# Kernel optimization log

Hardware: AMD Instinct MI355X
Metric: run time of the kernel (lower is better)

Reference implementation:

```python
import jax, jax.numpy as jnp
import numpy as np

DIM = 768
HEADS = 12
HEAD_DIM = DIM // HEADS  # 64, must equal 2*ROPE_DIM
HIDDEN = int(DIM * 4 * 2 / 3)  # 2048
EPS = 1e-6


def _ln(x, w, b, eps=EPS):
    mu = jnp.mean(x, -1, keepdims=True)
    var = jnp.mean((x - mu) ** 2, -1, keepdims=True)
    return (x - mu) * jax.lax.rsqrt(var + eps) * w + b


def _rotate_half(x):
    xr = x.reshape(x.shape[:-1] + (-1, 2))
    return jnp.stack((-xr[..., 1], xr[..., 0]), -1).reshape(x.shape)


def _rope_tables(H, W):
    # Matches get_rope: dim=32 per axis, pt_seq_len=16, theta=10000
    dim, pt, theta = 32, 16.0, 10000.0
    freqs = 1.0 / theta ** (np.arange(0, dim, 2, dtype=np.float32) / dim)  # [16]
    fH = np.repeat((np.arange(H, dtype=np.float32) / H * pt)[:, None] * freqs[None, :], 2, axis=-1)  # [H,32]
    fW = np.repeat((np.arange(W, dtype=np.float32) / W * pt)[:, None] * freqs[None, :], 2, axis=-1)  # [W,32]
    f = np.concatenate([np.broadcast_to(fH[:, None, :], (H, W, dim)),
                        np.broadcast_to(fW[None, :, :], (H, W, dim))], -1)  # [H,W,64]
    f = f.reshape(H * W, 2 * dim)
    return jnp.asarray(np.cos(f)), jnp.asarray(np.sin(f))


def block_forward(x, ln1_w, ln1_b, q_w, q_b, k_w, v_w, v_b, proj_w, proj_b,
                  ln2_w, ln2_b, w1_w, w1_b, w2_w, w2_b, ffn_w, ffn_b, w3_w, w3_b, ws):
    B, H, W, C = x.shape
    shortcut = x
    h = _ln(x, ln1_w, ln1_b)
    # window partition with padding
    pad_h = (-H) % ws
    pad_w = (-W) % ws
    h = jnp.pad(h, ((0, 0), (0, pad_h), (0, pad_w), (0, 0)))
    Hp, Wp = H + pad_h, W + pad_w
    h = h.reshape(B, Hp // ws, ws, Wp // ws, ws, C).transpose(0, 1, 3, 2, 4, 5).reshape(-1, ws, ws, C)
    Bw = h.shape[0]
    N = ws * ws
    t = h.reshape(Bw, N, C)
    q = t @ q_w + q_b  # k has no bias
    k = t @ k_w
    v = t @ v_w + v_b
    q = q.reshape(Bw, N, HEADS, HEAD_DIM).transpose(0, 2, 1, 3)  # [Bw,h,N,d]
    k = k.reshape(Bw, N, HEADS, HEAD_DIM).transpose(0, 2, 1, 3)
    v = v.reshape(Bw, N, HEADS, HEAD_DIM).transpose(0, 2, 1, 3)
    cos, sin = _rope_tables(ws, ws)  # [N, 64]
    q = q * cos + _rotate_half(q) * sin
    k = k * cos + _rotate_half(k) * sin
    scale = HEAD_DIM ** (-0.5)
    attn = jax.nn.softmax(jnp.einsum('bhnd,bhmd->bhnm', q * scale, k), axis=-1)
    o = jnp.einsum('bhnm,bhmd->bhnd', attn, v).transpose(0, 2, 1, 3).reshape(Bw, N, -1)
    o = o @ proj_w + proj_b
    o = o.reshape(Bw, ws, ws, C)
    # window unpartition
    o = o.reshape(B, Hp // ws, Wp // ws, ws, ws, C).transpose(0, 1, 3, 2, 4, 5).reshape(B, Hp, Wp, C)
    o = o[:, :H, :W, :]
    x = shortcut + o
    # SwiGLU MLP with sub-LN
    h = _ln(x, ln2_w, ln2_b)
    hid = jax.nn.silu(h @ w1_w + w1_b) * (h @ w2_w + w2_b)
    hid = _ln(hid, ffn_w, ffn_b)
    return x + hid @ w3_w + w3_b


def setup_inputs() -> dict:
    key = jax.random.key(0)
    ks = jax.random.split(key, 9)
    s = 0.02
    d = {
        'x': jax.random.normal(ks[0], (8, 64, 64, DIM), jnp.float32),
        'ln1_w': jnp.ones((DIM,), jnp.float32),
        'ln1_b': jnp.zeros((DIM,), jnp.float32),
        'q_w': jax.random.normal(ks[1], (DIM, DIM), jnp.float32) * s,
        'q_b': jnp.zeros((DIM,), jnp.float32),
        'k_w': jax.random.normal(ks[2], (DIM, DIM), jnp.float32) * s,
        'v_w': jax.random.normal(ks[3], (DIM, DIM), jnp.float32) * s,
        'v_b': jnp.zeros((DIM,), jnp.float32),
        'proj_w': jax.random.normal(ks[4], (DIM, DIM), jnp.float32) * s,
        'proj_b': jnp.zeros((DIM,), jnp.float32),
        'ln2_w': jnp.ones((DIM,), jnp.float32),
        'ln2_b': jnp.zeros((DIM,), jnp.float32),
        'w1_w': jax.random.normal(ks[5], (DIM, HIDDEN), jnp.float32) * s,
        'w1_b': jnp.zeros((HIDDEN,), jnp.float32),
        'w2_w': jax.random.normal(ks[6], (DIM, HIDDEN), jnp.float32) * s,
        'w2_b': jnp.zeros((HIDDEN,), jnp.float32),
        'ffn_w': jnp.ones((HIDDEN,), jnp.float32),
        'ffn_b': jnp.zeros((HIDDEN,), jnp.float32),
        'w3_w': jax.random.normal(ks[7], (HIDDEN, DIM), jnp.float32) * s,
        'w3_b': jnp.zeros((DIM,), jnp.float32),
        'window_size': 14,
    }
    return d


def reference(x, ln1_w, ln1_b, q_w, q_b, k_w, v_w, v_b, proj_w, proj_b,
              ln2_w, ln2_b, w1_w, w1_b, w2_w, w2_b, ffn_w, ffn_b, w3_w, w3_b, window_size):
    return block_forward(x, ln1_w, ln1_b, q_w, q_b, k_w, v_w, v_b, proj_w, proj_b,
                         ln2_w, ln2_b, w1_w, w1_b, w2_w, w2_b, ffn_w, ffn_b, w3_w, w3_b,
                         int(window_size))
```

## Files before the change

kernel.cpp:

```cpp
#include <hip/hip_runtime.h>
#include <hip/hip_bf16.h>
#include <stdint.h>

typedef unsigned short u16;
typedef unsigned int u32;
typedef __attribute__((ext_vector_type(4))) float f32x4;
typedef __attribute__((ext_vector_type(8))) short s16x8;
typedef __attribute__((ext_vector_type(4))) u32 u32x4;

#define DEV __device__ __forceinline__
#define AS1 __attribute__((address_space(1)))
#define AS3 __attribute__((address_space(3)))

constexpr int T2 = 8 * 64 * 64;
constexpr int C = 768;
constexpr int HID = 2048;
constexpr int CHUNK = 16384;
constexpr int QKVS = 2304;

DEV float blo(u32 u) { return __uint_as_float(u << 16); }
DEV float bhi(u32 u) { return __uint_as_float(u & 0xffff0000u); }
DEV u16 f2bf(float f) {
  u32 x = __float_as_uint(f);
  u32 r = x + 0x7fffu + ((x >> 16) & 1u);
  return (u16)(r >> 16);
}
DEV u32 pack2(float a, float b) { return (u32)f2bf(a) | ((u32)f2bf(b) << 16); }
DEV u32 cvtpk(float lo, float hi) {
  u32 r;
  asm("v_cvt_pk_bf16_f32 %0, %1, %2" : "=v"(r) : "v"(lo), "v"(hi));
  return r;
}

DEV void reduce2(float& s, float& q) {
#pragma unroll
  for (int o = 32; o > 0; o >>= 1) {
    s += __shfl_down(s, o);
    q += __shfl_down(q, o);
  }
  __shared__ float ps[8];
  int wave = threadIdx.x >> 6, lane = threadIdx.x & 63;
  if (lane == 0) { ps[wave] = s; ps[4 + wave] = q; }
  __syncthreads();
  s = ps[0] + ps[1] + ps[2] + ps[3];
  q = ps[4] + ps[5] + ps[6] + ps[7];
}

__global__ __launch_bounds__(256) void transpose_cvt_tiled_k(
    const float* __restrict__ src, u16* __restrict__ dst, int K, int N, int rs, int ro) {
  __shared__ float t[32][33];
  int k0 = blockIdx.x * 32, n0 = blockIdx.y * 32;
  int tx = threadIdx.x, ty = threadIdx.y;
#pragma unroll
  for (int j = 0; j < 4; ++j)
    t[ty + j * 8][tx] = src[(size_t)(k0 + ty + j * 8) * N + n0 + tx];
  __syncthreads();
#pragma unroll
  for (int j = 0; j < 4; ++j) {
    int n = n0 + ty + j * 8;
    dst[((size_t)n * rs + ro) * K + k0 + tx] = f2bf(t[tx][ty + j * 8]);
  }
}

__global__ void build_biases_k(const float* __restrict__ qb, const float* __restrict__ vbb,
                               const float* __restrict__ w1b, const float* __restrict__ w2b,
                               float* __restrict__ qkvb, float* __restrict__ w12b) {
  int i = blockIdx.x * 256 + threadIdx.x;
  if (i < 2304)
    qkvb[i] = i < 768 ? qb[i] : (i < 1536 ? 0.f : vbb[i - 1536]);
  int j = i - 2304;
  if (j >= 0 && j < 4096) w12b[j] = (j & 1) ? w2b[j >> 1] : w1b[j >> 1];
}

__global__ void rope_tables_k(float* __restrict__ ct, float* __restrict__ st) {
  int i = blockIdx.x * 256 + threadIdx.x;
  if (i >= 196 * 32) return;
  int n = i >> 5, jp = i & 31;
  int d = jp << 1;
  int r = n / 14, c = n - r * 14;
  float pos, fj;
  if (d < 32) { pos = (float)r * (16.f / 14.f); fj = (float)(d >> 1); }
  else        { pos = (float)c * (16.f / 14.f); fj = (float)((d - 32) >> 1); }
  float fr = __expf(fj * (-2.f / 32.f) * logf(10000.f));
  float ang = pos * fr;
  float cv = cosf(ang), sv = sinf(ang);
  ct[n * 64 + d] = cv; ct[n * 64 + d + 1] = cv;
  st[n * 64 + d] = sv; st[n * 64 + d + 1] = sv;
}

__global__ __launch_bounds__(256) void ln_k(const float* __restrict__ in,
    const float* __restrict__ w, const float* __restrict__ bb, u16* __restrict__ out) {
  size_t row = blockIdx.x;
  int tid = threadIdx.x;
  const float* xr = in + row * C;
  float v0 = xr[tid], v1 = xr[tid + 256], v2 = xr[tid + 512];
  float s = v0 + v1 + v2, q = v0 * v0 + v1 * v1 + v2 * v2;
  reduce2(s, q);
  float mu = s * (1.f / 768.f), var = q * (1.f / 768.f) - mu * mu;
  float rs = rsqrtf(var + 1e-6f);
  u16* orow = out + row * C;
  orow[tid]       = f2bf((v0 - mu) * rs * w[tid]       + bb[tid]);
  orow[tid + 256] = f2bf((v1 - mu) * rs * w[tid + 256] + bb[tid + 256]);
  orow[tid + 512] = f2bf((v2 - mu) * rs * w[tid + 512] + bb[tid + 512]);
}

DEV float rope1(float v, float p, int r, int d, bool odd, bool isq,
                const float* __restrict__ ct, const float* __restrict__ st) {
  int rem = r & 4095;
  int n = ((rem >> 6) % 14) * 14 + ((rem & 63) % 14);
  float c = ct[n * 64 + d], s = st[n * 64 + d];
  float o = odd ? (v * c + p * s) : (v * c - p * s);
  return isq ? o * 0.125f : o;
}

template <int EPI>
__global__ __launch_bounds__(256) void gemm_k(
    const u16* __restrict__ A, const u16* __restrict__ Bt,
    const float* __restrict__ bias, void* __restrict__ Cout,
    const float* __restrict__ resid, int M, int Nn, int K, int lda,
    const float* __restrict__ ct, const float* __restrict__ st) {
  __shared__ u16 As[128 * 64];
  __shared__ u16 Bs[128 * 64];
  const int tid = threadIdx.x;
  const int wave = tid >> 6, lane = tid & 63;
  const int wm = wave >> 1, wn = wave & 1;
  const int gx = gridDim.x;
  const int id = blockIdx.y * gx + blockIdx.x;
  const int xcd = id & 7;
  const int j0 = id >> 3;
  const int per_sub = gridDim.y << 4;
  const int sub = j0 / per_sub;
  const int jj = j0 - sub * per_sub;
  const int tm = xcd * (gx >> 3) + (sub << 4) + (jj & 15);
  const int tn = jj >> 4;
  const int l16 = lane & 15, lq = lane >> 4;

  f32x4 acc[4][4];
#pragma unroll
  for (int a = 0; a < 4; ++a)
#pragma unroll
    for (int b = 0; b < 4; ++b)
#pragma unroll
      for (int e = 0; e < 4; ++e) acc[a][b][e] = 0.f;

  const int nk = K >> 6;
  for (int kt = 0; kt < nk; ++kt) {
    const int k0 = kt << 6;
#pragma unroll
    for (int i = 0; i < 4; ++i) {
      int row = (((wave << 2) + i) << 3) + (lane >> 3);
      int cl = (lane & 7) ^ (row & 7);
      const u16* sa = A + (size_t)(tm * 128 + row) * lda + k0 + cl * 8;
      __builtin_amdgcn_global_load_lds((const AS1 u32*)sa,
          (AS3 u32*)(As + (((wave << 2) + i) << 9)), 16, 0, 0);
      const u16* sb = Bt + (size_t)(tn * 128 + row) * K + k0 + cl * 8;
      __builtin_amdgcn_global_load_lds((const AS1 u32*)sb,
          (AS3 u32*)(Bs + (((wave << 2) + i) << 9)), 16, 0, 0);
    }
    asm volatile("s_waitcnt vmcnt(0)" ::: "memory");
    __syncthreads();
#pragma unroll
    for (int ks = 0; ks < 2; ++ks) {
      s16x8 af[4], bfr[4];
#pragma unroll
      for (int mf = 0; mf < 4; ++mf) {
        int row = (wm << 6) + (mf << 4) + l16;
        int sc = ((ks << 2) + lq) ^ (row & 7);
        af[mf] = *(const s16x8*)(As + row * 64 + sc * 8);
      }
#pragma unroll
      for (int nf = 0; nf < 4; ++nf) {
        int row = (wn << 6) + (nf << 4) + l16;
        int sc = ((ks << 2) + lq) ^ (row & 7);
        bfr[nf] = *(const s16x8*)(Bs + row * 64 + sc * 8);
      }
      __builtin_amdgcn_s_setprio(1);
#pragma unroll
      for (int mf = 0; mf < 4; ++mf)
#pragma unroll
        for (int nf = 0; nf < 4; ++nf)
          acc[mf][nf] =
              __builtin_amdgcn_mfma_f32_16x16x32_bf16(af[mf], bfr[nf], acc[mf][nf], 0, 0, 0);
      __builtin_amdgcn_s_setprio(0);
    }
    __syncthreads();
  }

#pragma unroll
  for (int nf = 0; nf < 4; ++nf) {
    int col = (tn << 7) + (wn << 6) + (nf << 4) + l16;
    float bs = bias ? bias[col] : 0.f;
#pragma unroll
    for (int mf = 0; mf < 4; ++mf) {
      int rbase = (tm << 7) + (wm << 6) + (mf << 4) + (lq << 2);
      if constexpr (EPI == 0 || EPI == 3) {
        float v[4];
#pragma unroll
        for (int j = 0; j < 4; ++j) v[j] = acc[mf][nf][j] + bs;
        if constexpr (EPI == 3) {
          float pv[4];
#pragma unroll
          for (int j = 0; j < 4; ++j) pv[j] = __shfl_xor(v[j], 1);
          if (col < 1536) {
            bool odd = (l16 & 1) != 0, isq = col < 768;
            int d = col & 63;
#pragma unroll
            for (int j = 0; j < 4; ++j)
              v[j] = rope1(v[j], pv[j], rbase + j, d, odd, isq, ct, st);
          }
        }
        u32 p01 = cvtpk(v[0], v[1]);
        u32 p23 = cvtpk(v[2], v[3]);
        u16* cp = (u16*)Cout + (size_t)rbase * Nn + col;
        cp[0] = (u16)p01;
        cp[Nn] = (u16)(p01 >> 16);
        cp[2 * Nn] = (u16)p23;
        cp[3 * Nn] = (u16)(p23 >> 16);
      } else {
#pragma unroll
        for (int j = 0; j < 4; ++j) {
          size_t idx = (size_t)(rbase + j) * Nn + col;
          ((float*)Cout)[idx] = resid[idx] + acc[mf][nf][j] + bs;
        }
      }
    }
  }
}

__global__ __launch_bounds__(256) void attn_mfma_k(u16* __restrict__ qkv,
    const float* __restrict__ vb) {
  __shared__ u16 Vt[64 * 224];
  __shared__ u16 Pl[4 * 16 * 40];
  __shared__ int rowTab[208];
  int wid = blockIdx.x / 12, h = blockIdx.x - wid * 12;
  int bi = wid / 25, wr = wid - bi * 25;
  int hi = wr / 5, wj = wr - hi * 5;
  int rh = (hi == 4) ? 8 : 14, rw = (wj == 4) ? 8 : 14;
  int nv = rh * rw;
  int nk16 = (nv + 15) >> 4;
  int kvfull = nk16 >> 1;
  int nsteps = kvfull + (nk16 & 1);
  int vcols = ((nk16 + 1) >> 1) << 5;
  int tid = threadIdx.x;
  int rowbase = (bi * 64 + hi * 14) * 64 + wj * 14;

  if (tid < 208) {
    int mk = tid < nv ? tid : nv - 1;
    int nr = mk / rw, nc = mk - nr * rw;
    rowTab[tid] = rowbase + nr * 64 + nc;
  }
  __syncthreads();
  for (int idx = tid; idx < vcols * 32; idx += 256) {
    int key = idx >> 5, dp = idx & 31;
    int d = dp << 1;
    u32 val;
    if (key < nv) {
      size_t off = (size_t)rowTab[key] * QKVS + 1536 + (h << 6) + d;
      val = *(const u32*)(qkv + off);
    } else {
      val = pack2(vb[(h << 6) + d], vb[(h << 6) + d + 1]);
    }
    int b0 = (d * 448 + key * 2) ^ ((d & 7) << 4);
    int b1 = ((d + 1) * 448 + key * 2) ^ (((d + 1) & 7) << 4);
    Vt[b0 >> 1] = (u16)(val & 0xffffu);
    Vt[b1 >> 1] = (u16)(val >> 16);
  }
  __syncthreads();

  int wave = tid >> 6, lane = tid & 63;
  int l16 = lane & 15, lq = lane >> 4;
  u16* Pw = Pl + wave * 640;
  const u16* kbase = qkv + 768 + (h << 6);
  float vbr[4];
#pragma unroll
  for (int dt = 0; dt < 4; ++dt) vbr[dt] = vb[(h << 6) + dt * 16 + l16];

  int mtiles = (nv + 15) >> 4;
  for (int mt = wave; mt < mtiles; mt += 4) {
    s16x8 a[2];
    {
      int qi = mt * 16 + l16;
      const u16* qp = qkv + (size_t)rowTab[qi] * QKVS + (h << 6);
      a[0] = *(const s16x8*)(qp + lq * 8);
      a[1] = *(const s16x8*)(qp + 32 + lq * 8);
    }
    f32x4 O[4];
#pragma unroll
    for (int dt = 0; dt < 4; ++dt)
#pragma unroll
      for (int j = 0; j < 4; ++j) O[dt][j] = 0.f;
    float lrow[4] = {0.f, 0.f, 0.f, 0.f};

    for (int kv = 0; kv < nsteps; ++kv) {
      const bool full = kv < kvfull;
      const int keyb = kv << 5;
      f32x4 s0 = {0.f, 0.f, 0.f, 0.f}, s1 = {0.f, 0.f, 0.f, 0.f};
      int key0 = keyb + l16, key1 = key0 + 16;
      const u16* kr0 = kbase + (size_t)rowTab[key0] * QKVS;
      const u16* kr1 = full ? (kbase + (size_t)rowTab[key1] * QKVS) : kbase;
      __builtin_amdgcn_s_setprio(1);
#pragma unroll
      for (int s = 0; s < 2; ++s) {
        s16x8 b0 = *(const s16x8*)(kr0 + s * 32 + lq * 8);
        s0 = __builtin_amdgcn_mfma_f32_16x16x32_bf16(a[s], b0, s0, 0, 0, 0);
        if (full) {
          s16x8 b1 = *(const s16x8*)(kr1 + s * 32 + lq * 8);
          s1 = __builtin_amdgcn_mfma_f32_16x16x32_bf16(a[s], b1, s1, 0, 0, 0);
        }
      }
      __builtin_amdgcn_s_setprio(0);
#pragma unroll
      for (int j = 0; j < 4; ++j) {
        float p0 = key0 < nv ? __expf(s0[j]) : (key0 < 196 ? 1.f : 0.f);
        float p1 = full ? (key1 < nv ? __expf(s1[j]) : (key1 < 196 ? 1.f : 0.f)) : 0.f;
        float rs = p0 + p1;
        rs += __shfl_xor(rs, 1);
        rs += __shfl_xor(rs, 2);
        rs += __shfl_xor(rs, 4);
        rs += __shfl_xor(rs, 8);
        lrow[j] += rs;
        u32 pk = cvtpk(p0, p1);
        Pw[(lq * 4 + j) * 40 + l16] = (u16)pk;
        Pw[(lq * 4 + j) * 40 + l16 + 16] = (u16)(pk >> 16);
      }
      s16x8 pa = *(const s16x8*)(Pw + l16 * 40 + lq * 8);
      __builtin_amdgcn_s_setprio(1);
#pragma unroll
      for (int dt = 0; dt < 4; ++dt) {
        int d = dt * 16 + l16;
        int vbyte = (d * 448 + keyb * 2 + lq * 16) ^ ((d & 7) << 4);
        s16x8 bv = *(const s16x8*)(Vt + (vbyte >> 1));
        O[dt] = __builtin_amdgcn_mfma_f32_16x16x32_bf16(pa, bv, O[dt], 0, 0, 0);
      }
      __builtin_amdgcn_s_setprio(0);
    }
    int Prem = 196 - (nk16 << 4);
    if (Prem > 0) {
#pragma unroll
      for (int j = 0; j < 4; ++j) {
        lrow[j] += (float)Prem;
#pragma unroll
        for (int dt = 0; dt < 4; ++dt) O[dt][j] += (float)Prem * vbr[dt];
      }
    }
#pragma unroll
    for (int j = 0; j < 4; ++j) {
      int qi = mt * 16 + lq * 4 + j;
      if (qi < nv) {
        float inv = 1.f / lrow[j];
        u16* op = qkv + (size_t)rowTab[qi] * QKVS + (h << 6);
#pragma unroll
        for (int dt = 0; dt < 4; ++dt) op[dt * 16 + l16] = f2bf(O[dt][j] * inv);
      }
    }
  }
}

__global__ __launch_bounds__(256) void swiglu_ln_k(u16* __restrict__ h12,
    const float* __restrict__ w, const float* __restrict__ bb) {
  size_t row = blockIdx.x;
  int tid = threadIdx.x;
  const u32x4 ua = *(const u32x4*)(h12 + row * 4096 + tid * 16);
  const u32x4 ub = *(const u32x4*)(h12 + row * 4096 + tid * 16 + 8);
  u32 pp[8] = {ua.x, ua.y, ua.z, ua.w, ub.x, ub.y, ub.z, ub.w};
  float g[8];
  float s = 0.f, qq = 0.f;
#pragma unroll
  for (int j = 0; j < 8; ++j) {
    float a = blo(pp[j]), b = bhi(pp[j]);
    float sl = a / (1.f + __expf(-a));
    g[j] = sl * b;
    s += g[j];
    qq += g[j] * g[j];
  }
  reduce2(s, qq);
  float mu = s * (1.f / 2048.f);
  float var = qq * (1.f / 2048.f) - mu * mu;
  float rs = rsqrtf(var + 1e-6f);
  const float* wp = w + tid * 8;
  const float* bp = bb + tid * 8;
  u32 o4[4];
#pragma unroll
  for (int j = 0; j < 4; ++j) {
    float o0 = (g[2 * j] - mu) * rs * wp[2 * j] + bp[2 * j];
    float o1 = (g[2 * j + 1] - mu) * rs * wp[2 * j + 1] + bp[2 * j + 1];
    o4[j] = cvtpk(o0, o1);
  }
  *(u32x4*)(h12 + row * 4096 + tid * 8) = (u32x4){o4[0], o4[1], o4[2], o4[3]};
}

extern "C" void kernel_launch(void* const* d_in, const int* in_sizes, int n_in,
                              void* d_out, int out_size, void* d_ws, size_t ws_size,
                              hipStream_t stream) {
  const float* x    = (const float*)d_in[0];
  const float* ln1w = (const float*)d_in[1];
  const float* ln1b = (const float*)d_in[2];
  const float* qw   = (const float*)d_in[3];
  const float* qb   = (const float*)d_in[4];
  const float* kw   = (const float*)d_in[5];
  const float* vw   = (const float*)d_in[6];
  const float* vb   = (const float*)d_in[7];
  const float* pw   = (const float*)d_in[8];
  const float* pb   = (const float*)d_in[9];
  const float* ln2w = (const float*)d_in[10];
  const float* ln2b = (const float*)d_in[11];
  const float* w1   = (const float*)d_in[12];
  const float* w1b  = (const float*)d_in[13];
  const float* w2   = (const float*)d_in[14];
  const float* w2b  = (const float*)d_in[15];
  const float* ffw  = (const float*)d_in[16];
  const float* ffb  = (const float*)d_in[17];
  const float* w3   = (const float*)d_in[18];
  const float* w3b  = (const float*)d_in[19];

  char* ws = (char*)d_ws;
  size_t off = 0;
  auto alloc = [&](size_t bytes) -> char* {
    char* p = ws + off;
    off += (bytes + 255) & ~(size_t)255;
    return p;
  };
  u16* qkvwt = (u16*)alloc((size_t)QKVS * 768 * 2);
  u16* pwt   = (u16*)alloc((size_t)768 * 768 * 2);
  u16* w12t  = (u16*)alloc((size_t)4096 * 768 * 2);
  u16* w3t   = (u16*)alloc((size_t)768 * 2048 * 2);
  float* qkvb = (float*)alloc((size_t)QKVS * 4);
  float* w12b = (float*)alloc((size_t)4096 * 4);
  float* ct = (float*)alloc((size_t)196 * 64 * 4);
  float* st = (float*)alloc((size_t)196 * 64 * 4);
  u16* xw  = (u16*)alloc((size_t)T2 * C * 2);
  u16* qkv = (u16*)alloc((size_t)T2 * QKVS * 2);
  u16* h12c = qkv;
  float* x2 = (float*)d_out;

  dim3 tb(32, 8);
  transpose_cvt_tiled_k<<<dim3(24, 24), tb, 0, stream>>>(qw, qkvwt, 768, 768, 1, 0);
  transpose_cvt_tiled_k<<<dim3(24, 24), tb, 0, stream>>>(kw, qkvwt + (size_t)768 * 768, 768, 768, 1, 0);
  transpose_cvt_tiled_k<<<dim3(24, 24), tb, 0, stream>>>(vw, qkvwt + (size_t)1536 * 768, 768, 768, 1, 0);
  transpose_cvt_tiled_k<<<dim3(24, 24), tb, 0, stream>>>(pw, pwt, 768, 768, 1, 0);
  transpose_cvt_tiled_k<<<dim3(24, 64), tb, 0, stream>>>(w1, w12t, 768, 2048, 2, 0);
  transpose_cvt_tiled_k<<<dim3(24, 64), tb, 0, stream>>>(w2, w12t, 768, 2048, 2, 1);
  transpose_cvt_tiled_k<<<dim3(64, 24), tb, 0, stream>>>(w3, w3t, 2048, 768, 1, 0);
  build_biases_k<<<25, 256, 0, stream>>>(qb, vb, w1b, w2b, qkvb, w12b);
  rope_tables_k<<<(196 * 32 + 255) / 256, 256, 0, stream>>>(ct, st);

  ln_k<<<T2, 256, 0, stream>>>(x, ln1w, ln1b, xw);
  gemm_k<3><<<dim3(T2 / 128, QKVS / 128), 256, 0, stream>>>(
      xw, qkvwt, qkvb, qkv, nullptr, T2, QKVS, 768, 768, ct, st);
  attn_mfma_k<<<200 * 12, 256, 0, stream>>>(qkv, vb);
  gemm_k<2><<<dim3(T2 / 128, 6), 256, 0, stream>>>(
      qkv, pwt, pb, x2, x, T2, 768, 768, QKVS, nullptr, nullptr);

  ln_k<<<T2, 256, 0, stream>>>(x2, ln2w, ln2b, xw);
  for (int cidx = 0; cidx < T2 / CHUNK; ++cidx) {
    const u16* hrow = xw + (size_t)cidx * CHUNK * C;
    gemm_k<0><<<dim3(CHUNK / 128, 32), 256, 0, stream>>>(
        hrow, w12t, w12b, h12c, nullptr, CHUNK, 4096, 768, 768, nullptr, nullptr);
    swiglu_ln_k<<<CHUNK, 256, 0, stream>>>(h12c, ffw, ffb);
    gemm_k<2><<<dim3(CHUNK / 128, 6), 256, 0, stream>>>(
        h12c, w3t, w3b, x2 + (size_t)cidx * CHUNK * C,
        x2 + (size_t)cidx * CHUNK * C, CHUNK, 768, 2048, 4096, nullptr, nullptr);
  }
}
```

Before: 1.075 ms.

## Store post-attention residual in bf16, halve FFN chunk, nontemporal epilogue stores

The projection GEMM now writes the residual sum x2 as bf16 instead of fp32. A new bf16 LayerNorm kernel (384 threads) reads it, and the final GEMM reads the bf16 residual and writes fp32 output with nontemporal stores. FFN chunk size drops from 16384 to 8192 so the intermediate fits beside h2 in the qkv buffer, and the GEMM tile-swizzle groups shrink from 16 to 8 rows. This cuts fp32 residual traffic and may improve cache locality, at the cost of bf16 rounding on the residual stream and more kernel launches.

```diff
diff --git a/kernel.cpp b/kernel.cpp
--- a/kernel.cpp
+++ b/kernel.cpp
@@ -15,11 +15,12 @@
 constexpr int T2 = 8 * 64 * 64;
 constexpr int C = 768;
 constexpr int HID = 2048;
-constexpr int CHUNK = 16384;
+constexpr int CHUNK = 8192;
 constexpr int QKVS = 2304;
 
 DEV float blo(u32 u) { return __uint_as_float(u << 16); }
 DEV float bhi(u32 u) { return __uint_as_float(u & 0xffff0000u); }
+DEV float b2f(u16 u) { return __uint_as_float((u32)u << 16); }
 DEV u16 f2bf(float f) {
   u32 x = __float_as_uint(f);
   u32 r = x + 0x7fffu + ((x >> 16) & 1u);
@@ -32,18 +33,20 @@
   return r;
 }
 
+template <int NW>
 DEV void reduce2(float& s, float& q) {
 #pragma unroll
   for (int o = 32; o > 0; o >>= 1) {
     s += __shfl_down(s, o);
     q += __shfl_down(q, o);
   }
-  __shared__ float ps[8];
+  __shared__ float ps[2 * NW];
   int wave = threadIdx.x >> 6, lane = threadIdx.x & 63;
-  if (lane == 0) { ps[wave] = s; ps[4 + wave] = q; }
+  if (lane == 0) { ps[wave] = s; ps[NW + wave] = q; }
   __syncthreads();
-  s = ps[0] + ps[1] + ps[2] + ps[3];
-  q = ps[4] + ps[5] + ps[6] + ps[7];
+  s = 0.f; q = 0.f;
+#pragma unroll
+  for (int i = 0; i < NW; ++i) { s += ps[i]; q += ps[NW + i]; }
 }
 
 __global__ __launch_bounds__(256) void transpose_cvt_tiled_k(
@@ -95,13 +98,28 @@
   const float* xr = in + row * C;
   float v0 = xr[tid], v1 = xr[tid + 256], v2 = xr[tid + 512];
   float s = v0 + v1 + v2, q = v0 * v0 + v1 * v1 + v2 * v2;
-  reduce2(s, q);
+  reduce2<4>(s, q);
   float mu = s * (1.f / 768.f), var = q * (1.f / 768.f) - mu * mu;
   float rs = rsqrtf(var + 1e-6f);
   u16* orow = out + row * C;
   orow[tid]       = f2bf((v0 - mu) * rs * w[tid]       + bb[tid]);
   orow[tid + 256] = f2bf((v1 - mu) * rs * w[tid + 256] + bb[tid + 256]);
   orow[tid + 512] = f2bf((v2 - mu) * rs * w[tid + 512] + bb[tid + 512]);
+}
+
+__global__ __launch_bounds__(384) void ln_bf16_k(const u16* __restrict__ in,
+    const float* __restrict__ w, const float* __restrict__ bb, u16* __restrict__ out) {
+  size_t row = blockIdx.x;
+  int t = threadIdx.x;
+  u32 u = ((const u32*)(in + row * C))[t];
+  float v0 = blo(u), v1 = bhi(u);
+  float s = v0 + v1, q = v0 * v0 + v1 * v1;
+  reduce2<6>(s, q);
+  float mu = s * (1.f / 768.f), var = q * (1.f / 768.f) - mu * mu;
+  float rs = rsqrtf(var + 1e-6f);
+  float o0 = (v0 - mu) * rs * w[2 * t] + bb[2 * t];
+  float o1 = (v1 - mu) * rs * w[2 * t + 1] + bb[2 * t + 1];
+  ((u32*)(out + row * C))[t] = cvtpk(o0, o1);
 }
 
 DEV float rope1(float v, float p, int r, int d, bool odd, bool isq,
@@ -117,7 +135,7 @@
 __global__ __launch_bounds__(256) void gemm_k(
     const u16* __restrict__ A, const u16* __restrict__ Bt,
     const float* __restrict__ bias, void* __restrict__ Cout,
-    const float* __restrict__ resid, int M, int Nn, int K, int lda,
+    const void* __restrict__ resid, int M, int Nn, int K, int lda,
     const float* __restrict__ ct, const float* __restrict__ st) {
   __shared__ u16 As[128 * 64];
   __shared__ u16 Bs[128 * 64];
@@ -128,11 +146,12 @@
   const int id = blockIdx.y * gx + blockIdx.x;
   const int xcd = id & 7;
   const int j0 = id >> 3;
-  const int per_sub = gridDim.y << 4;
+  const int W = gx >> 3;
+  const int per_sub = gridDim.y << 3;
   const int sub = j0 / per_sub;
   const int jj = j0 - sub * per_sub;
-  const int tm = xcd * (gx >> 3) + (sub << 4) + (jj & 15);
-  const int tn = jj >> 4;
+  const int tm = xcd * W + (sub << 3) + (jj & 7);
+  const int tn = jj >> 3;
   const int l16 = lane & 15, lq = lane >> 4;
 
   f32x4 acc[4][4];
@@ -193,10 +212,23 @@
 #pragma unroll
     for (int mf = 0; mf < 4; ++mf) {
       int rbase = (tm << 7) + (wm << 6) + (mf << 4) + (lq << 2);
-      if constexpr (EPI == 0 || EPI == 3) {
+      if constexpr (EPI == 2) {
+        const u16* rp = (const u16*)resid;
+#pragma unroll
+        for (int j = 0; j < 4; ++j) {
+          size_t idx = (size_t)(rbase + j) * Nn + col;
+          __builtin_nontemporal_store(
+              b2f(rp[idx]) + acc[mf][nf][j] + bs, (float*)Cout + idx);
+        }
+      } else {
         float v[4];
 #pragma unroll
         for (int j = 0; j < 4; ++j) v[j] = acc[mf][nf][j] + bs;
+        if constexpr (EPI == 1) {
+          const float* rp = (const float*)resid;
+#pragma unroll
+          for (int j = 0; j < 4; ++j) v[j] += rp[(size_t)(rbase + j) * Nn + col];
+        }
         if constexpr (EPI == 3) {
           float pv[4];
 #pragma unroll
@@ -212,16 +244,10 @@
         u32 p01 = cvtpk(v[0], v[1]);
         u32 p23 = cvtpk(v[2], v[3]);
         u16* cp = (u16*)Cout + (size_t)rbase * Nn + col;
-        cp[0] = (u16)p01;
-        cp[Nn] = (u16)(p01 >> 16);
-        cp[2 * Nn] = (u16)p23;
-        cp[3 * Nn] = (u16)(p23 >> 16);
-      } else {
-#pragma unroll
-        for (int j = 0; j < 4; ++j) {
-          size_t idx = (size_t)(rbase + j) * Nn + col;
-          ((float*)Cout)[idx] = resid[idx] + acc[mf][nf][j] + bs;
-        }
+        __builtin_nontemporal_store((u16)p01, cp);
+        __builtin_nontemporal_store((u16)(p01 >> 16), cp + Nn);
+        __builtin_nontemporal_store((u16)p23, cp + 2 * Nn);
+        __builtin_nontemporal_store((u16)(p23 >> 16), cp + 3 * Nn);
       }
     }
   }
@@ -373,7 +399,7 @@
     s += g[j];
     qq += g[j] * g[j];
   }
-  reduce2(s, qq);
+  reduce2<4>(s, qq);
   float mu = s * (1.f / 2048.f);
   float var = qq * (1.f / 2048.f) - mu * mu;
   float rs = rsqrtf(var + 1e-6f);
@@ -430,8 +456,10 @@
   float* st = (float*)alloc((size_t)196 * 64 * 4);
   u16* xw  = (u16*)alloc((size_t)T2 * C * 2);
   u16* qkv = (u16*)alloc((size_t)T2 * QKVS * 2);
-  u16* h12c = qkv;
-  float* x2 = (float*)d_out;
+  u16* x2b  = xw;
+  u16* h2   = qkv;
+  u16* h12c = qkv + (size_t)T2 * C;
+  float* outp = (float*)d_out;
 
   dim3 tb(32, 8);
   transpose_cvt_tiled_k<<<dim3(24, 24), tb, 0, stream>>>(qw, qkvwt, 768, 768, 1, 0);
@@ -448,17 +476,17 @@
   gemm_k<3><<<dim3(T2 / 128, QKVS / 128), 256, 0, stream>>>(
       xw, qkvwt, qkvb, qkv, nullptr, T2, QKVS, 768, 768, ct, st);
   attn_mfma_k<<<200 * 12, 256, 0, stream>>>(qkv, vb);
-  gemm_k<2><<<dim3(T2 / 128, 6), 256, 0, stream>>>(
-      qkv, pwt, pb, x2, x, T2, 768, 768, QKVS, nullptr, nullptr);
-
-  ln_k<<<T2, 256, 0, stream>>>(x2, ln2w, ln2b, xw);
+  gemm_k<1><<<dim3(T2 / 128, 6), 256, 0, stream>>>(
+      qkv, pwt, pb, x2b, x, T2, 768, 768, QKVS, nullptr, nullptr);
+
+  ln_bf16_k<<<T2, 384, 0, stream>>>(x2b, ln2w, ln2b, h2);
   for (int cidx = 0; cidx < T2 / CHUNK; ++cidx) {
-    const u16* hrow = xw + (size_t)cidx * CHUNK * C;
+    const u16* hrow = h2 + (size_t)cidx * CHUNK * C;
     gemm_k<0><<<dim3(CHUNK / 128, 32), 256, 0, stream>>>(
         hrow, w12t, w12b, h12c, nullptr, CHUNK, 4096, 768, 768, nullptr, nullptr);
     swiglu_ln_k<<<CHUNK, 256, 0, stream>>>(h12c, ffw, ffb);
     gemm_k<2><<<dim3(CHUNK / 128, 6), 256, 0, stream>>>(
-        h12c, w3t, w3b, x2 + (size_t)cidx * CHUNK * C,
-        x2 + (size_t)cidx * CHUNK * C, CHUNK, 768, 2048, 4096, nullptr, nullptr);
-  }
-}
+        h12c, w3t, w3b, outp + (size_t)cidx * CHUNK * C,
+        x2b + (size_t)cidx * CHUNK * C, CHUNK, 768, 2048, 4096, nullptr, nullptr);
+  }
+}
```

Result: slower. 1.233 ms (+14.8%).
